# Kernel optimization log

Hardware: AMD Instinct MI355X
Metric: run time of the kernel (lower is better)

## Reference

```python
import jax, jax.numpy as jnp
import numpy as np

B, W_DIM, CIN, COUT, K, H = 16, 512, 512, 512, 3, 64
PAD = (K - 1) // 2          # conv padding, also filtered_lrelu padding
GAIN = float(np.sqrt(2.0))  # lrelu gain (not torgb)
SLOPE = 0.2                 # lrelu slope (not torgb)
CLAMP = 256.0               # conv_clamp
AFFINE_WG = float(1.0 / np.sqrt(W_DIM))  # FullyConnectedLayer weight_gain


def setup_inputs() -> dict:
    key = jax.random.key(0)
    k0, k1, k2, k3 = jax.random.split(key, 4)
    return {
        "x": jax.random.normal(k0, (B, CIN, H, H), jnp.float32),
        "w": jax.random.normal(k1, (B, W_DIM), jnp.float32),
        "affine_weight": jax.random.normal(k2, (CIN, W_DIM), jnp.float32),
        "affine_bias": jnp.ones((CIN,), jnp.float32),       # bias_init=1
        "conv_weight": jax.random.normal(k3, (COUT, CIN, K, K), jnp.float32),
        "bias": jnp.zeros((COUT,), jnp.float32),
        "magnitude_ema": jnp.ones((), jnp.float32),
    }


def reference(x, w, affine_weight, affine_bias, conv_weight, bias, magnitude_ema):
    input_gain = jax.lax.rsqrt(magnitude_ema)
    # --- affine (FullyConnectedLayer, linear act, lr_mult=1) ---
    s = w @ (affine_weight * AFFINE_WG).T + affine_bias          # [B, CIN]
    # --- modulated_conv2d with demodulation (is_torgb=False) ---
    wk = conv_weight * jax.lax.rsqrt(
        jnp.mean(jnp.square(conv_weight), axis=(1, 2, 3), keepdims=True))
    s = s * jax.lax.rsqrt(jnp.mean(jnp.square(s)))
    wb = wk[None] * s[:, None, :, None, None]                    # [B,COUT,CIN,K,K]
    dcoefs = jax.lax.rsqrt(jnp.sum(jnp.square(wb), axis=(2, 3, 4)) + 1e-8)  # [B,COUT]
    wb = wb * dcoefs[:, :, None, None, None] * input_gain
    # grouped conv: groups = batch, one weight set per sample
    xg = x.reshape(1, B * CIN, H, H)
    wg = wb.reshape(B * COUT, CIN, K, K)
    y = jax.lax.conv_general_dilated(
        xg, wg, window_strides=(1, 1), padding=[(PAD, PAD), (PAD, PAD)],
        dimension_numbers=("NCHW", "OIHW", "NCHW"), feature_group_count=B)
    y = y.reshape(B, COUT, H, H)
    # --- filtered_lrelu: up=down=1, fu=fd=None (identity FIR) ---
    # => bias add, zero-pad by `padding`, lrelu * gain, clamp
    y = y + bias[:, None, None]
    y = jnp.pad(y, ((0, 0), (0, 0), (PAD, PAD), (PAD, PAD)))
    y = jnp.where(y >= 0, y, y * SLOPE) * GAIN
    y = jnp.clip(y, -CLAMP, CLAMP)                               # [B,COUT,66,66]
    return y
```

## Files before the change

### kernel.cpp

```cpp
#include <hip/hip_runtime.h>

#define B_     16
#define WDIM   512
#define CIN_   512
#define COUT_  512
#define HH     64
#define KC     32
#define NCHUNK (CIN_/KC)
#define AFFINE_WG 0.044194173824159216f
#define GAIN_  1.4142135623730951f
#define CLAMP_ 256.0f

#define WBYTES 36864
#define XROWB  4224
#define XBYTES (10 * XROWB)

typedef __attribute__((ext_vector_type(4))) float f32x4;
typedef __attribute__((ext_vector_type(8))) short bf16x8;
typedef __attribute__((ext_vector_type(8))) unsigned short u16x8;

__device__ __forceinline__ unsigned short f2bf(float f) {
    union { float f; unsigned u; } un; un.f = f;
    unsigned u = un.u;
    u += 0x7FFFu + ((u >> 16) & 1u);
    return (unsigned short)(u >> 16);
}

__device__ __forceinline__ void gl_lds16(const void* g, void* l) {
    __builtin_amdgcn_global_load_lds(
        reinterpret_cast<const __attribute__((address_space(1))) unsigned int*>(
            reinterpret_cast<uintptr_t>(g)),
        reinterpret_cast<__attribute__((address_space(3))) unsigned int*>(
            reinterpret_cast<uintptr_t>(l)),
        16, 0, 0);
}


__global__ void k_affine(const float* __restrict__ w, const float* __restrict__ aw,
                         const float* __restrict__ ab, float* __restrict__ s,
                         float* __restrict__ part) {
    const int tid = threadIdx.x;
    const int b = blockIdx.x >> 1;
    const int c = ((blockIdx.x & 1) << 8) + tid;
    const f32x4* wr = (const f32x4*)(w + (size_t)b * WDIM);
    const f32x4* ar = (const f32x4*)(aw + (size_t)c * WDIM);
    float acc = 0.f;
    #pragma unroll 4
    for (int k = 0; k < WDIM / 4; ++k) {
        f32x4 a = ar[k], bb = wr[k];
        acc += a[0]*bb[0] + a[1]*bb[1] + a[2]*bb[2] + a[3]*bb[3];
    }
    float sv = acc * AFFINE_WG + ab[c];
    s[b * CIN_ + c] = sv;
    __shared__ float red[256];
    red[tid] = sv * sv;
    __syncthreads();
    for (int off = 128; off > 0; off >>= 1) {
        if (tid < off) red[tid] += red[tid + off];
        __syncthreads();
    }
    if (tid == 0) part[blockIdx.x] = red[0];
}

__global__ void k_wnorm(const float* __restrict__ cw, float* __restrict__ alpha,
                        float* __restrict__ Q) {
    const int o = blockIdx.x;
    const int tid = threadIdx.x;
    __shared__ float qsh[512];
    __shared__ float red[256];
    __shared__ float a_sh;
    float tot = 0.f;
    #pragma unroll
    for (int half = 0; half < 2; ++half) {
        const int c = tid + half * 256;
        const float* p = cw + ((size_t)o * 512 + c) * 9;
        float qs = 0.f;
        #pragma unroll
        for (int t = 0; t < 9; ++t) { float v = p[t]; qs += v * v; }
        qsh[c] = qs; tot += qs;
    }
    red[tid] = tot; __syncthreads();
    for (int off = 128; off > 0; off >>= 1) {
        if (tid < off) red[tid] += red[tid + off];
        __syncthreads();
    }
    if (tid == 0) { a_sh = rsqrtf(red[0] * (1.0f / 4608.0f)); alpha[o] = a_sh; }
    __syncthreads();
    const float a2 = a_sh * a_sh;
    Q[(size_t)o * 512 + tid]       = a2 * qsh[tid];
    Q[(size_t)o * 512 + tid + 256] = a2 * qsh[tid + 256];
}

__global__ void k_g(const float* __restrict__ s, const float* __restrict__ part,
                    const float* __restrict__ Q, const float* __restrict__ alpha,
                    const float* __restrict__ ema, float* __restrict__ g) {
    const int tid = threadIdx.x;
    const int b = blockIdx.x >> 1;
    const int o = ((blockIdx.x & 1) << 8) + tid;
    __shared__ float rs2_sh;
    if (tid == 0) {
        float t = 0.f;
        #pragma unroll
        for (int i = 0; i < 32; ++i) t += part[i];
        rs2_sh = 8192.0f / t;
    }
    __syncthreads();
    const f32x4* sh = (const f32x4*)(s + (size_t)b * CIN_);
    const f32x4* qq = (const f32x4*)(Q + (size_t)o * CIN_);
    float d = 0.f;
    #pragma unroll 4
    for (int k = 0; k < CIN_ / 4; ++k) {
        f32x4 a = sh[k], q4 = qq[k];
        d += a[0]*a[0]*q4[0] + a[1]*a[1]*q4[1] + a[2]*a[2]*q4[2] + a[3]*a[3]*q4[3];
    }
    const float ig = rsqrtf(ema[0]);
    g[b * COUT_ + o] = alpha[o] * rsqrtf(d * rs2_sh + 1e-8f) * ig;
}

__global__ void k_wprep2(const float* __restrict__ cw, unsigned short* __restrict__ wb) {
    const int S = blockIdx.x * 256 + threadIdx.x;
    const int p    = S / 2304;
    const int srem = S - p * 2304;
    const int a    = srem * 16;
    const int tap  = a >> 12;
    const int o    = (a >> 6) & 63;
    const int c0   = ((a & 63) ^ ((o & 6) << 3)) >> 1;
    const int ot = p >> 4, cc = p & 15;
    const int og = ot * 64 + o;
    const int cg = cc * 32 + c0;
    const float* src = cw + ((size_t)og * 512 + cg) * 9 + tap;
    u16x8 v;
    #pragma unroll
    for (int j = 0; j < 8; ++j) v[j] = f2bf(src[j * 9]);
    *(u16x8*)(wb + (size_t)S * 8) = v;
}

__global__ void k_xprep2(const float* __restrict__ x, const float* __restrict__ s,
                         const float* __restrict__ part, unsigned short* __restrict__ xbf) {
    __shared__ float rs_sh;
    __shared__ char tile[8 * 4096];
    const int tid = threadIdx.x;
    if (tid == 0) {
        float t = 0.f;
        #pragma unroll
        for (int i = 0; i < 32; ++i) t += part[i];
        rs_sh = rsqrtf(t * (1.0f / 8192.0f));
    }
    __syncthreads();
    const float rs = rs_sh;
    const int blk = blockIdx.x;
    const int b  = blk >> 7;
    const int cc = (blk >> 3) & 15;
    const int rg = blk & 7;
    const int c   = tid >> 3;
    const int k8  = tid & 7;
    const float sc = s[b * CIN_ + cc * 32 + c] * rs;
    const float* src = x + (((size_t)(b * CIN_ + cc * 32 + c)) * HH + rg * 8) * HH + k8 * 8;
    #pragma unroll
    for (int row = 0; row < 8; ++row) {
        const f32x4 v0 = *(const f32x4*)(src + (size_t)row * HH);
        const f32x4 v1 = *(const f32x4*)(src + (size_t)row * HH + 4);
        #pragma unroll
        for (int q = 0; q < 8; ++q) {
            const float v = (q < 4) ? v0[q] : v1[q - 4];
            const int col = k8 * 8 + q + 1;
            const int byte = ((col * 64 + 2 * c) ^ ((col & 6) << 3)) - 64;
            *(unsigned short*)(tile + row * 4096 + byte) = f2bf(v * sc);
        }
    }
    __syncthreads();
    unsigned short* dst = xbf + ((size_t)(b * 16 + cc) * 64 + rg * 8) * 2048;
    const u16x8* tsrc = (const u16x8*)tile;
    #pragma unroll
    for (int k = 0; k < 8; ++k)
        *(u16x8*)(dst + (size_t)(tid + k * 256) * 8) = tsrc[tid + k * 256];
}

__global__ __launch_bounds__(512, 2) void k_conv9(
    const unsigned short* __restrict__ xbf, const unsigned short* __restrict__ wb,
    const float* __restrict__ g, const float* __restrict__ bias,
    float* __restrict__ out) {
    __shared__ char Wl[WBYTES];
    __shared__ char Xl[XBYTES];

    const int tid  = threadIdx.x;
    const int lane = tid & 63;
    const int wv   = tid >> 6;
    const int l15  = lane & 15;
    const int hi   = lane >> 4;

    const int orig = blockIdx.x;
    const int wg = (orig & 7) * 128 + (orig >> 3);
    const int b  = wg >> 6;
    const int ot = (wg >> 3) & 7;
    const int rt = wg & 7;
    const int h0 = rt * 8;

    const f32x4 zero4 = {0.f, 0.f, 0.f, 0.f};
    f32x4 acc[4][4];
    #pragma unroll
    for (int i = 0; i < 4; ++i)
        #pragma unroll
        for (int j = 0; j < 4; ++j) acc[i][j] = zero4;

    {
        unsigned int* x0 = (unsigned int*)Xl;
        for (int i = tid; i < XBYTES / 4; i += 512) x0[i] = 0u;
    }
    __syncthreads();

    const char* wsrc0 = (const char*)wb + (size_t)ot * 16 * WBYTES;
    const char* xsrc0 = (const char*)xbf + (size_t)b * 16 * 262144;

    #pragma unroll 1
    for (int cc = 0; cc < NCHUNK; ++cc) {
        if (tid < 256) {
            const char* wsrc = wsrc0 + (size_t)cc * WBYTES;
            #pragma unroll
            for (int r = 0; r < 9; ++r)
                gl_lds16(wsrc + r * 4096 + tid * 16, Wl + r * 4096 + tid * 16);
        } else {
            const int t2 = tid - 256;
            const char* xsrc = xsrc0 + (size_t)cc * 262144;
            #pragma unroll
            for (int r = 0; r < 10; ++r) {
                const int h_in = h0 - 1 + r;
                if ((unsigned)h_in < 64u)
                    gl_lds16(xsrc + (size_t)h_in * 4096 + t2 * 16,
                             Xl + r * XROWB + 64 + t2 * 16);
            }
        }
        __syncthreads();

        #pragma unroll
        for (int tap = 0; tap < 9; ++tap) {
            const int ti = tap / 3, tj = tap - ti * 3;
            bf16x8 af[4];
            #pragma unroll
            for (int mi = 0; mi < 4; ++mi) {
                const int o = mi * 16 + l15;
                int byte = (tap << 12) + (o << 6) + (hi << 4);
                byte ^= ((o & 6) << 3);
                af[mi] = *(const bf16x8*)(Wl + byte);
            }
            bf16x8 bg[4];
            const int row = wv + ti;
            #pragma unroll
            for (int ni = 0; ni < 4; ++ni) {
                const int col = ni * 16 + l15 + tj;
                int byte = (((row * 66 + col) << 5) + (hi << 3)) << 1;
                byte ^= ((col & 6) << 3);
                bg[ni] = *(const bf16x8*)(Xl + byte);
            }
            __builtin_amdgcn_s_setprio(1);
            #pragma unroll
            for (int mi = 0; mi < 4; ++mi)
                #pragma unroll
                for (int ni = 0; ni < 4; ++ni)
                    acc[mi][ni] = __builtin_amdgcn_mfma_f32_16x16x32_bf16(
                        af[mi], bg[ni], acc[mi][ni], 0, 0, 0);
            __builtin_amdgcn_s_setprio(0);
        }
        if (cc != NCHUNK - 1) __syncthreads();
    }

    {
        const int obase = ot * 64;
        const int orow = h0 + wv + 1;
        #pragma unroll
        for (int mi = 0; mi < 4; ++mi) {
            #pragma unroll
            for (int r = 0; r < 4; ++r) {
                const int o = obase + mi * 16 + hi * 4 + r;
                const float gg = g[b * COUT_ + o];
                const float bb = bias[o];
                float* op = out + ((size_t)(b * COUT_ + o) * 66 + orow) * 66;
                #pragma unroll
                for (int ni = 0; ni < 4; ++ni) {
                    float v = acc[mi][ni][r] * gg + bb;
                    v = (v >= 0.f ? v : v * 0.2f) * GAIN_;
                    v = fminf(fmaxf(v, -CLAMP_), CLAMP_);
                    op[ni * 16 + l15 + 1] = v;
                }
                if (l15 == 0)  op[0]  = 0.f;
                if (l15 == 15) op[65] = 0.f;
            }
        }
        if (rt == 0 || rt == 7) {
            const int row = (rt == 0) ? 0 : 65;
            for (int i = tid; i < 64 * 66; i += 512) {
                const int o = obase + i / 66, col = i - (i / 66) * 66;
                out[((size_t)(b * COUT_ + o) * 66 + row) * 66 + col] = 0.f;
            }
        }
    }
}

extern "C" void kernel_launch(void* const* d_in, const int* in_sizes, int n_in,
                              void* d_out, int out_size, void* d_ws, size_t ws_size,
                              hipStream_t stream) {
    const float* x    = (const float*)d_in[0];
    const float* w    = (const float*)d_in[1];
    const float* aw   = (const float*)d_in[2];
    const float* ab   = (const float*)d_in[3];
    const float* cw   = (const float*)d_in[4];
    const float* bias = (const float*)d_in[5];
    const float* ema  = (const float*)d_in[6];
    float* out = (float*)d_out;

    float* wsf   = (float*)d_ws;
    float* s     = wsf;
    float* part  = wsf + 8192;
    float* alpha = wsf + 16512;
    float* Q     = wsf + 17024;
    float* g     = wsf + 279168;
    unsigned short* wb  = (unsigned short*)((char*)d_ws + 1179648);
    unsigned short* xbf = (unsigned short*)((char*)d_ws + 5898240);

    k_affine <<<32, 256, 0, stream>>>(w, aw, ab, s, part);
    k_wnorm  <<<512, 256, 0, stream>>>(cw, alpha, Q);
    k_g      <<<32, 256, 0, stream>>>(s, part, Q, alpha, ema, g);
    k_wprep2 <<<1152, 256, 0, stream>>>(cw, wb);
    k_xprep2 <<<2048, 256, 0, stream>>>(x, s, part, xbf);
    k_conv9  <<<1024, 512, 0, stream>>>(xbf, wb, g, bias, out);
}
```

Before: 356.1 us.

## Halve conv row tile to four rows and coalesce weight prep via LDS

```diff
diff --git a/kernel.cpp b/kernel.cpp
--- a/kernel.cpp
+++ b/kernel.cpp
@@ -11,10 +11,6 @@
 #define GAIN_  1.4142135623730951f
 #define CLAMP_ 256.0f
 
-#define WBYTES 36864
-#define XROWB  4224
-#define XBYTES (10 * XROWB)
-
 typedef __attribute__((ext_vector_type(4))) float f32x4;
 typedef __attribute__((ext_vector_type(8))) short bf16x8;
 typedef __attribute__((ext_vector_type(8))) unsigned short u16x8;
@@ -117,22 +113,32 @@
     g[b * COUT_ + o] = alpha[o] * rsqrtf(d * rs2_sh + 1e-8f) * ig;
 }
 
-__global__ void k_wprep2(const float* __restrict__ cw, unsigned short* __restrict__ wb) {
-    const int S = blockIdx.x * 256 + threadIdx.x;
-    const int p    = S / 2304;
-    const int srem = S - p * 2304;
-    const int a    = srem * 16;
-    const int tap  = a >> 12;
-    const int o    = (a >> 6) & 63;
-    const int c0   = ((a & 63) ^ ((o & 6) << 3)) >> 1;
+__global__ void k_wprep5(const float* __restrict__ cw, unsigned short* __restrict__ wb) {
+    __shared__ char tile[36864];
+    const int tid = threadIdx.x;
+    const int p = blockIdx.x;
     const int ot = p >> 4, cc = p & 15;
-    const int og = ot * 64 + o;
-    const int cg = cc * 32 + c0;
-    const float* src = cw + ((size_t)og * 512 + cg) * 9 + tap;
-    u16x8 v;
-    #pragma unroll
-    for (int j = 0; j < 8; ++j) v[j] = f2bf(src[j * 9]);
-    *(u16x8*)(wb + (size_t)S * 8) = v;
+    const float* base = cw + ((size_t)(ot * 64) * 512 + cc * 32) * 9;
+    #pragma unroll
+    for (int k = 0; k < 18; ++k) {
+        const int lin4 = tid + k * 256;
+        const int row  = lin4 / 72;
+        const int i4   = lin4 - row * 72;
+        const f32x4 v = *(const f32x4*)(base + (size_t)row * 4608 + i4 * 4);
+        #pragma unroll
+        for (int j = 0; j < 4; ++j) {
+            const int e   = i4 * 4 + j;
+            const int c   = e / 9;
+            const int tap = e - c * 9;
+            const int byte = ((tap * 2048 + row * 32 + c) << 1) ^ ((row & 6) << 3);
+            *(unsigned short*)(tile + byte) = f2bf(v[j]);
+        }
+    }
+    __syncthreads();
+    u16x8* dst = (u16x8*)(wb + (size_t)p * 18432);
+    const u16x8* src = (const u16x8*)tile;
+    #pragma unroll
+    for (int k = 0; k < 9; ++k) dst[tid + k * 256] = src[tid + k * 256];
 }
 
 __global__ void k_xprep2(const float* __restrict__ x, const float* __restrict__ s,
@@ -176,25 +182,22 @@
         *(u16x8*)(dst + (size_t)(tid + k * 256) * 8) = tsrc[tid + k * 256];
 }
 
-__global__ __launch_bounds__(512, 2) void k_conv9(
+__global__ __launch_bounds__(256, 2) void k_conv2b(
     const unsigned short* __restrict__ xbf, const unsigned short* __restrict__ wb,
     const float* __restrict__ g, const float* __restrict__ bias,
     float* __restrict__ out) {
-    __shared__ char Wl[WBYTES];
-    __shared__ char Xl[XBYTES];
+    __shared__ unsigned short Wlds[9 * 64 * 32];
+    __shared__ unsigned short Xlds[6 * 66 * 32];
 
     const int tid  = threadIdx.x;
     const int lane = tid & 63;
     const int wv   = tid >> 6;
     const int l15  = lane & 15;
     const int hi   = lane >> 4;
-
-    const int orig = blockIdx.x;
-    const int wg = (orig & 7) * 128 + (orig >> 3);
-    const int b  = wg >> 6;
-    const int ot = (wg >> 3) & 7;
-    const int rt = wg & 7;
-    const int h0 = rt * 8;
+    const int b  = blockIdx.z;
+    const int ot = blockIdx.y;
+    const int rt = blockIdx.x;
+    const int h0 = rt * 4;
 
     const f32x4 zero4 = {0.f, 0.f, 0.f, 0.f};
     f32x4 acc[4][4];
@@ -204,31 +207,27 @@
         for (int j = 0; j < 4; ++j) acc[i][j] = zero4;
 
     {
-        unsigned int* x0 = (unsigned int*)Xl;
-        for (int i = tid; i < XBYTES / 4; i += 512) x0[i] = 0u;
-    }
-    __syncthreads();
-
-    const char* wsrc0 = (const char*)wb + (size_t)ot * 16 * WBYTES;
+        unsigned int* p = (unsigned int*)Xlds;
+        for (int i = tid; i < 6 * 66 * 32 / 2; i += 256) p[i] = 0u;
+    }
+    __syncthreads();
+
+    const char* wsrc0 = (const char*)wb + (size_t)ot * 16 * 36864;
     const char* xsrc0 = (const char*)xbf + (size_t)b * 16 * 262144;
 
-    #pragma unroll 1
     for (int cc = 0; cc < NCHUNK; ++cc) {
-        if (tid < 256) {
-            const char* wsrc = wsrc0 + (size_t)cc * WBYTES;
-            #pragma unroll
-            for (int r = 0; r < 9; ++r)
-                gl_lds16(wsrc + r * 4096 + tid * 16, Wl + r * 4096 + tid * 16);
-        } else {
-            const int t2 = tid - 256;
-            const char* xsrc = xsrc0 + (size_t)cc * 262144;
-            #pragma unroll
-            for (int r = 0; r < 10; ++r) {
-                const int h_in = h0 - 1 + r;
-                if ((unsigned)h_in < 64u)
-                    gl_lds16(xsrc + (size_t)h_in * 4096 + t2 * 16,
-                             Xl + r * XROWB + 64 + t2 * 16);
-            }
+        const char* wsrc = wsrc0 + (size_t)cc * 36864;
+        #pragma unroll
+        for (int r = 0; r < 9; ++r)
+            gl_lds16(wsrc + r * 4096 + tid * 16,
+                     (char*)Wlds + r * 4096 + wv * 1024);
+        const char* xsrc = xsrc0 + (size_t)cc * 262144;
+        #pragma unroll
+        for (int r = 0; r < 6; ++r) {
+            const int h_in = h0 - 1 + r;
+            if ((unsigned)h_in < 64u)
+                gl_lds16(xsrc + (size_t)h_in * 4096 + tid * 16,
+                         (char*)Xlds + r * 4224 + 64 + wv * 1024);
         }
         __syncthreads();
 
@@ -241,7 +240,7 @@
                 const int o = mi * 16 + l15;
                 int byte = (tap << 12) + (o << 6) + (hi << 4);
                 byte ^= ((o & 6) << 3);
-                af[mi] = *(const bf16x8*)(Wl + byte);
+                af[mi] = *(const bf16x8*)((const char*)Wlds + byte);
             }
             bf16x8 bg[4];
             const int row = wv + ti;
@@ -250,16 +249,14 @@
                 const int col = ni * 16 + l15 + tj;
                 int byte = (((row * 66 + col) << 5) + (hi << 3)) << 1;
                 byte ^= ((col & 6) << 3);
-                bg[ni] = *(const bf16x8*)(Xl + byte);
+                bg[ni] = *(const bf16x8*)((const char*)Xlds + byte);
             }
-            __builtin_amdgcn_s_setprio(1);
             #pragma unroll
             for (int mi = 0; mi < 4; ++mi)
                 #pragma unroll
                 for (int ni = 0; ni < 4; ++ni)
                     acc[mi][ni] = __builtin_amdgcn_mfma_f32_16x16x32_bf16(
                         af[mi], bg[ni], acc[mi][ni], 0, 0, 0);
-            __builtin_amdgcn_s_setprio(0);
         }
         if (cc != NCHUNK - 1) __syncthreads();
     }
@@ -286,9 +283,9 @@
                 if (l15 == 15) op[65] = 0.f;
             }
         }
-        if (rt == 0 || rt == 7) {
+        if (rt == 0 || rt == 15) {
             const int row = (rt == 0) ? 0 : 65;
-            for (int i = tid; i < 64 * 66; i += 512) {
+            for (int i = tid; i < 64 * 66; i += 256) {
                 const int o = obase + i / 66, col = i - (i / 66) * 66;
                 out[((size_t)(b * COUT_ + o) * 66 + row) * 66 + col] = 0.f;
             }
@@ -320,7 +317,7 @@
     k_affine <<<32, 256, 0, stream>>>(w, aw, ab, s, part);
     k_wnorm  <<<512, 256, 0, stream>>>(cw, alpha, Q);
     k_g      <<<32, 256, 0, stream>>>(s, part, Q, alpha, ema, g);
-    k_wprep2 <<<1152, 256, 0, stream>>>(cw, wb);
+    k_wprep5 <<<128, 256, 0, stream>>>(cw, wb);
     k_xprep2 <<<2048, 256, 0, stream>>>(x, s, part, xbf);
-    k_conv9  <<<1024, 512, 0, stream>>>(xbf, wb, g, bias, out);
-}
+    k_conv2b <<<dim3(16, 8, 16), 256, 0, stream>>>(xbf, wb, g, bias, out);
+}
```

After: 334.7 us. 6.0% less time.
